# Performance work log

Hardware: AMD Instinct MI355X
Metric: run time of the kernel (lower is better)

The kernel has to match this reference:

```python
import jax, jax.numpy as jnp
import numpy as np

N = 50000
E = 1600000
D = 128
BN_EPS = 1e-5


def setup_inputs() -> dict:
    key = jax.random.key(0)
    ks = jax.random.split(key, 6)
    feature = jax.random.normal(ks[0], (N, D), dtype=jnp.float32)
    snorm_n = jax.random.uniform(ks[1], (N, 1), dtype=jnp.float32)
    src = jax.random.randint(ks[2], (E,), 0, N, dtype=jnp.int64)
    dst = jax.random.randint(ks[3], (E,), 0, N, dtype=jnp.int64)
    W = jax.random.normal(ks[4], (D, D), dtype=jnp.float32) * (1.0 / np.sqrt(D))
    b = jax.random.normal(ks[5], (D,), dtype=jnp.float32) * 0.01
    gamma = jnp.ones((D,), dtype=jnp.float32)
    beta = jnp.zeros((D,), dtype=jnp.float32)
    return {"feature": feature, "snorm_n": snorm_n, "src": src, "dst": dst,
            "W": W, "b": b, "gamma": gamma, "beta": beta}


def reference(feature, snorm_n, src, dst, W, b, gamma, beta):
    # --- copy_src + mean reduce (DGL update_all) ---
    msg = feature[src]                                    # [E, D] gather
    agg = jax.ops.segment_sum(msg, dst, num_segments=N)   # [N, D] scatter-add
    deg = jax.ops.segment_sum(jnp.ones((src.shape[0],), feature.dtype), dst,
                              num_segments=N)             # [N]
    has_msg = deg > 0
    mean = agg / jnp.maximum(deg, 1.0)[:, None]
    # nodes with no incoming edges keep their original 'h' (DGL semantics)
    h = jnp.where(has_msg[:, None], mean, feature)
    # --- apply_nodes: linear ---
    h = h @ W.T + b
    # --- graph norm ---
    h = h * snorm_n
    # --- batch norm (training-mode stats, biased variance, eps=1e-5) ---
    mu = jnp.mean(h, axis=0)
    var = jnp.mean((h - mu) ** 2, axis=0)
    h = (h - mu) / jnp.sqrt(var + BN_EPS) * gamma + beta
    # --- activation + residual (dropout p=0 -> identity) ---
    h = jax.nn.relu(h)
    h = feature + h
    return h
```

## Files before the change

### kernel.cpp

```cpp
#include <hip/hip_runtime.h>

#define D 128
#define BN_EPS 1e-5f
#define ROWS 16
#define CHUNK 4096
#define CAP_SCAN 512

typedef unsigned int u32;
typedef unsigned short u16;

__device__ inline u32 pk_bf16(float x, float y) {
    u32 ux = __float_as_uint(x), uy = __float_as_uint(y);
    ux = (ux + 0x7fffu + ((ux >> 16) & 1u)) >> 16;
    uy = (uy + 0x7fffu + ((uy >> 16) & 1u)) >> 16;
    return ux | (uy << 16);
}

__global__ __launch_bounds__(256) void cast_transpose(const float* __restrict__ feat,
                                                      u16* __restrict__ feat16,
                                                      const float* __restrict__ W,
                                                      float* __restrict__ Wt,
                                                      int ncast) {
    int b = blockIdx.x;
    if (b < ncast) {
        size_t i = ((size_t)b * 256 + threadIdx.x) * 8;
        float4 f0 = *reinterpret_cast<const float4*>(feat + i);
        float4 f1 = *reinterpret_cast<const float4*>(feat + i + 4);
        uint4 o;
        o.x = pk_bf16(f0.x, f0.y);
        o.y = pk_bf16(f0.z, f0.w);
        o.z = pk_bf16(f1.x, f1.y);
        o.w = pk_bf16(f1.z, f1.w);
        *reinterpret_cast<uint4*>(feat16 + i) = o;
    } else {
        int i = (b - ncast) * 256 + threadIdx.x;
        int r = i >> 7, c = i & 127;
        Wt[c * D + r] = W[i];
    }
}

__global__ __launch_bounds__(256) void passA(const int* __restrict__ dst,
                                             int* __restrict__ blkcnt,
                                             int nch, int nedges) {
    __shared__ int cnt[256];
    cnt[threadIdx.x] = 0;
    __syncthreads();
    const int e0 = blockIdx.x * CHUNK;
    for (int r = 0; r < CHUNK / 256; ++r) {
        int e = e0 + r * 256 + threadIdx.x;
        if (e < nedges) atomicAdd(&cnt[dst[e] >> 8], 1);
    }
    __syncthreads();
    blkcnt[(size_t)threadIdx.x * nch + blockIdx.x] = cnt[threadIdx.x];
}

__global__ __launch_bounds__(CAP_SCAN) void scanB1(int* __restrict__ blkcnt,
                                                   int* __restrict__ gtot,
                                                   int nch) {
    __shared__ int s[CAP_SCAN];
    const int t = threadIdx.x;
    const size_t row = (size_t)blockIdx.x * nch;
    int v = (t < nch) ? blkcnt[row + t] : 0;
    s[t] = v;
    __syncthreads();
    for (int off = 1; off < CAP_SCAN; off <<= 1) {
        int u = (t >= off) ? s[t - off] : 0;
        __syncthreads();
        s[t] += u;
        __syncthreads();
    }
    if (t < nch) blkcnt[row + t] = s[t] - v;
    if (t == 0) gtot[blockIdx.x] = s[CAP_SCAN - 1];
}

__global__ __launch_bounds__(256) void scanB2(const int* __restrict__ gtot,
                                              int* __restrict__ bucket_base,
                                              int* __restrict__ bucket_cnt) {
    __shared__ int s[256];
    const int t = threadIdx.x;
    int v = gtot[t];
    s[t] = v;
    __syncthreads();
    for (int off = 1; off < 256; off <<= 1) {
        int u = (t >= off) ? s[t - off] : 0;
        __syncthreads();
        s[t] += u;
        __syncthreads();
    }
    bucket_base[t] = s[t] - v;
    bucket_cnt[t] = v;
}

__global__ __launch_bounds__(256) void passB(const int* __restrict__ src,
                                             const int* __restrict__ dst,
                                             const int* __restrict__ blkcnt,
                                             const int* __restrict__ bucket_base,
                                             u32* __restrict__ gpacked,
                                             int nch, int nedges) {
    __shared__ int cnt[256];
    __shared__ int gbase[256];
    const int t = threadIdx.x;
    gbase[t] = blkcnt[(size_t)t * nch + blockIdx.x] + bucket_base[t];
    cnt[t] = 0;
    __syncthreads();
    const int e0 = blockIdx.x * CHUNK;
    for (int r = 0; r < CHUNK / 256; ++r) {
        int e = e0 + r * 256 + t;
        if (e < nedges) {
            int d = dst[e];
            int b = d >> 8;
            int pos = atomicAdd(&cnt[b], 1);
            gpacked[gbase[b] + pos] = (u32)src[e] | ((u32)(d & 255) << 16);
        }
    }
}

__global__ __launch_bounds__(256) void pass2(const u32* __restrict__ gpacked,
                                             const int* __restrict__ bucket_base,
                                             const int* __restrict__ bucket_cnt,
                                             u16* __restrict__ epos,
                                             int* __restrict__ count,
                                             int* __restrict__ offs,
                                             int nnodes) {
    __shared__ int cnt[256], lo[256], cur[256];
    const int t = threadIdx.x;
    const int b = blockIdx.x;
    const int nE = bucket_cnt[b];
    const int base = bucket_base[b];
    cnt[t] = 0;
    __syncthreads();
    for (int i = t; i < nE; i += 256) atomicAdd(&cnt[gpacked[base + i] >> 16], 1);
    __syncthreads();
    int v = cnt[t];
    lo[t] = v;
    __syncthreads();
    for (int off = 1; off < 256; off <<= 1) {
        int u = (t >= off) ? lo[t - off] : 0;
        __syncthreads();
        lo[t] += u;
        __syncthreads();
    }
    int excl = lo[t] - v;
    int n = (b << 8) + t;
    if (n < nnodes) { count[n] = v; offs[n] = base + excl; }
    cur[t] = excl;
    __syncthreads();
    for (int i = t; i < nE; i += 256) {
        u32 p = gpacked[base + i];
        int pos = atomicAdd(&cur[p >> 16], 1);
        epos[base + pos] = (u16)(p & 0xffffu);
    }
}

__global__ __launch_bounds__(256, 6) void fused_agg_linear(
        const float* __restrict__ feat,
        const u16* __restrict__ feat16,
        const float* __restrict__ snorm,
        const int* __restrict__ offs,
        const int* __restrict__ count,
        const u16* __restrict__ epos,
        const float* __restrict__ Wt,
        const float* __restrict__ bias,
        float* __restrict__ y,
        float* __restrict__ partial) {
    __shared__ float hs[ROWS][D];
    const int row0 = blockIdx.x * ROWS;
    const int wid = threadIdx.x >> 6;
    const int lane = threadIdx.x & 63;
    const int q = lane >> 4;
    const int ql = lane & 15;

#define LDB(s) (*reinterpret_cast<const uint4*>(feat16 + (size_t)(s) * D + 8 * ql))
#define ADD8(a, u) { \
    a[0] += __uint_as_float((u).x << 16); a[1] += __uint_as_float((u).x & 0xffff0000u); \
    a[2] += __uint_as_float((u).y << 16); a[3] += __uint_as_float((u).y & 0xffff0000u); \
    a[4] += __uint_as_float((u).z << 16); a[5] += __uint_as_float((u).z & 0xffff0000u); \
    a[6] += __uint_as_float((u).w << 16); a[7] += __uint_as_float((u).w & 0xffff0000u); }

    for (int rr = 0; rr < 4; ++rr) {
        const int r = wid * 4 + rr;
        const int n = row0 + r;
        const int dg = count[n];
        const int o = offs[n];
        float a0[8], a1[8];
        #pragma unroll
        for (int k = 0; k < 8; ++k) { a0[k] = 0.0f; a1[k] = 0.0f; }

        for (int base = 0; base < dg; base += 64) {
            const int m = min(64, dg - base);
            int myidx = (lane < m) ? (int)epos[o + base + lane] : 0;
            int j = 0;
            for (; j + 8 <= m; j += 8) {
                int s0 = __shfl(myidx, j + q, 64);
                int s1 = __shfl(myidx, j + 4 + q, 64);
                uint4 u0 = LDB(s0);
                uint4 u1 = LDB(s1);
                ADD8(a0, u0);
                ADD8(a1, u1);
            }
            if (j + 4 <= m) {
                int s0 = __shfl(myidx, j + q, 64);
                uint4 u0 = LDB(s0);
                ADD8(a0, u0);
                j += 4;
            }
            int rem = m - j;
            if (rem) {
                int s0 = __shfl(myidx, j + (q < rem ? q : 0), 64);
                if (q < rem) { uint4 u0 = LDB(s0); ADD8(a1, u0); }
            }
        }

        float av[8];
        #pragma unroll
        for (int k = 0; k < 8; ++k) {
            float v = a0[k] + a1[k];
            v += __shfl_xor(v, 16, 64);
            v += __shfl_xor(v, 32, 64);
            av[k] = v;
        }
        if (dg > 0) {
            float inv = 1.0f / (float)dg;
            #pragma unroll
            for (int k = 0; k < 8; ++k) av[k] *= inv;
        } else {
            float4 f0 = *reinterpret_cast<const float4*>(feat + (size_t)n * D + 8 * ql);
            float4 f1 = *reinterpret_cast<const float4*>(feat + (size_t)n * D + 8 * ql + 4);
            av[0] = f0.x; av[1] = f0.y; av[2] = f0.z; av[3] = f0.w;
            av[4] = f1.x; av[5] = f1.y; av[6] = f1.z; av[7] = f1.w;
        }
        if (q == 0) {
            *reinterpret_cast<float4*>(&hs[r][8 * ql]) = make_float4(av[0], av[1], av[2], av[3]);
            *reinterpret_cast<float4*>(&hs[r][8 * ql + 4]) = make_float4(av[4], av[5], av[6], av[7]);
        }
    }
#undef LDB
#undef ADD8
    __syncthreads();

    const int d = threadIdx.x & 127;
    const int half2 = threadIdx.x >> 7;
    float acc[8];
    #pragma unroll
    for (int r = 0; r < 8; ++r) acc[r] = 0.0f;

    for (int k = 0; k < D; k += 4) {
        float w0 = Wt[(k + 0) * D + d];
        float w1 = Wt[(k + 1) * D + d];
        float w2 = Wt[(k + 2) * D + d];
        float w3 = Wt[(k + 3) * D + d];
        #pragma unroll
        for (int r = 0; r < 8; ++r) {
            float4 h4 = *reinterpret_cast<const float4*>(&hs[half2 * 8 + r][k]);
            acc[r] += h4.x * w0 + h4.y * w1 + h4.z * w2 + h4.w * w3;
        }
    }

    const float bb = bias[d];
    float psum = 0.0f, psq = 0.0f;
    #pragma unroll
    for (int r = 0; r < 8; ++r) {
        const int n = row0 + half2 * 8 + r;
        float v = (acc[r] + bb) * snorm[n];
        y[(size_t)n * D + d] = v;
        psum += v;
        psq += v * v;
    }
    __syncthreads();
    if (half2 == 1) { hs[0][d] = psum; hs[1][d] = psq; }
    __syncthreads();
    if (half2 == 0) {
        psum += hs[0][d];
        psq += hs[1][d];
        partial[(size_t)blockIdx.x * 256 + d] = psum;
        partial[(size_t)blockIdx.x * 256 + 128 + d] = psq;
    }
}

__global__ __launch_bounds__(256) void bn_reduce(const float* __restrict__ partial,
                                                 const float* __restrict__ gamma,
                                                 const float* __restrict__ beta,
                                                 float* __restrict__ bnparam,
                                                 int nchunk, float inv_n) {
    const int d = blockIdx.x;
    float s = 0.0f, q = 0.0f;
    for (int b = threadIdx.x; b < nchunk; b += 256) {
        s += partial[(size_t)b * 256 + d];
        q += partial[(size_t)b * 256 + 128 + d];
    }
    for (int off = 32; off > 0; off >>= 1) {
        s += __shfl_down(s, off, 64);
        q += __shfl_down(q, off, 64);
    }
    __shared__ float ss[4], qq[4];
    int wid = threadIdx.x >> 6;
    int lane = threadIdx.x & 63;
    if (lane == 0) { ss[wid] = s; qq[wid] = q; }
    __syncthreads();
    if (threadIdx.x == 0) {
        float S = ss[0] + ss[1] + ss[2] + ss[3];
        float Q = qq[0] + qq[1] + qq[2] + qq[3];
        float mu = S * inv_n;
        float var = Q * inv_n - mu * mu;
        var = fmaxf(var, 0.0f);
        float rstd = rsqrtf(var + BN_EPS);
        float scale = gamma[d] * rstd;
        float shift = beta[d] - mu * scale;
        bnparam[d] = scale;
        bnparam[D + d] = shift;
    }
}

__global__ __launch_bounds__(256) void finalize(const float* __restrict__ feat,
                                                float* __restrict__ y,
                                                const float* __restrict__ bnparam,
                                                int total4) {
    int i = blockIdx.x * 256 + threadIdx.x;
    if (i >= total4) return;
    int c = i & 31;
    float4 v = reinterpret_cast<float4*>(y)[i];
    float4 f = reinterpret_cast<const float4*>(feat)[i];
    float4 sc = reinterpret_cast<const float4*>(bnparam)[c];
    float4 sh = reinterpret_cast<const float4*>(bnparam + D)[c];
    v.x = f.x + fmaxf(v.x * sc.x + sh.x, 0.0f);
    v.y = f.y + fmaxf(v.y * sc.y + sh.y, 0.0f);
    v.z = f.z + fmaxf(v.z * sc.z + sh.z, 0.0f);
    v.w = f.w + fmaxf(v.w * sc.w + sh.w, 0.0f);
    reinterpret_cast<float4*>(y)[i] = v;
}

extern "C" void kernel_launch(void* const* d_in, const int* in_sizes, int n_in,
                              void* d_out, int out_size, void* d_ws, size_t ws_size,
                              hipStream_t stream) {
    const float* feat  = (const float*)d_in[0];
    const float* snorm = (const float*)d_in[1];
    const int*   src   = (const int*)d_in[2];
    const int*   dst   = (const int*)d_in[3];
    const float* W     = (const float*)d_in[4];
    const float* bias  = (const float*)d_in[5];
    const float* gamma = (const float*)d_in[6];
    const float* beta  = (const float*)d_in[7];

    const int N = in_sizes[1];
    const int E = in_sizes[2];
    const int nblk = N / ROWS;
    const int nch = (E + CHUNK - 1) / CHUNK;
    const int nbuck = (N + 255) >> 8;
    const int ncast = (N * D) / (8 * 256);

    int* count       = (int*)d_ws;
    int* offs        = count + N;
    int* blkcnt      = offs + N;
    int* gtot        = blkcnt + (size_t)256 * nch;
    int* bucket_base = gtot + 256;
    int* bucket_cnt  = bucket_base + 256;
    u32* gpacked     = (u32*)(bucket_cnt + 256);
    u16* epos        = (u16*)(gpacked + E);
    u16* feat16      = epos + E;
    float* Wt        = (float*)(feat16 + (size_t)N * D);
    float* partial   = Wt + D * D;
    float* bnparam   = partial + (size_t)nblk * 256;

    float* y = (float*)d_out;

    cast_transpose<<<ncast + 64, 256, 0, stream>>>(feat, feat16, W, Wt, ncast);

    passA<<<nch, 256, 0, stream>>>(dst, blkcnt, nch, E);
    scanB1<<<256, CAP_SCAN, 0, stream>>>(blkcnt, gtot, nch);
    scanB2<<<1, 256, 0, stream>>>(gtot, bucket_base, bucket_cnt);
    passB<<<nch, 256, 0, stream>>>(src, dst, blkcnt, bucket_base, gpacked, nch, E);
    pass2<<<nbuck, 256, 0, stream>>>(gpacked, bucket_base, bucket_cnt,
                                     epos, count, offs, N);

    fused_agg_linear<<<nblk, 256, 0, stream>>>(feat, feat16, snorm, offs, count,
                                               epos, Wt, bias, y, partial);

    bn_reduce<<<D, 256, 0, stream>>>(partial, gamma, beta, bnparam,
                                     nblk, 1.0f / (float)N);

    {
        int total4 = N * D / 4;
        finalize<<<(total4 + 255) / 256, 256, 0, stream>>>(feat, y, bnparam, total4);
    }
}
```

Before: 159.1 us.

## Fuse bucket counting into prep kernel, widen sort passes, unroll gather further

Merges the destination-bucket counting pass into the cast/transpose kernel so one launch does both, removing a kernel boundary. Doubles the edge chunk size and halves the scan block, and runs passB and pass2 with 512 threads per block. Widens the gather loop in the aggregation kernel to four independent accumulators, putting more loads in flight per wave. The extra accumulators raise register pressure under the existing occupancy bound.

```diff
diff --git a/kernel.cpp b/kernel.cpp
--- a/kernel.cpp
+++ b/kernel.cpp
@@ -3,8 +3,8 @@
 #define D 128
 #define BN_EPS 1e-5f
 #define ROWS 16
-#define CHUNK 4096
-#define CAP_SCAN 512
+#define CHUNK 8192
+#define CAP_SCAN 256
 
 typedef unsigned int u32;
 typedef unsigned short u16;
@@ -16,12 +16,15 @@
     return ux | (uy << 16);
 }
 
-__global__ __launch_bounds__(256) void cast_transpose(const float* __restrict__ feat,
-                                                      u16* __restrict__ feat16,
-                                                      const float* __restrict__ W,
-                                                      float* __restrict__ Wt,
-                                                      int ncast) {
-    int b = blockIdx.x;
+__global__ __launch_bounds__(256) void prep(const float* __restrict__ feat,
+                                            u16* __restrict__ feat16,
+                                            const float* __restrict__ W,
+                                            float* __restrict__ Wt,
+                                            const int* __restrict__ dst,
+                                            int* __restrict__ blkcnt,
+                                            int ncast, int nch, int nedges) {
+    __shared__ int cnt[256];
+    const int b = blockIdx.x;
     if (b < ncast) {
         size_t i = ((size_t)b * 256 + threadIdx.x) * 8;
         float4 f0 = *reinterpret_cast<const float4*>(feat + i);
@@ -32,26 +35,22 @@
         o.z = pk_bf16(f1.x, f1.y);
         o.w = pk_bf16(f1.z, f1.w);
         *reinterpret_cast<uint4*>(feat16 + i) = o;
-    } else {
+    } else if (b < ncast + 64) {
         int i = (b - ncast) * 256 + threadIdx.x;
         int r = i >> 7, c = i & 127;
         Wt[c * D + r] = W[i];
-    }
-}
-
-__global__ __launch_bounds__(256) void passA(const int* __restrict__ dst,
-                                             int* __restrict__ blkcnt,
-                                             int nch, int nedges) {
-    __shared__ int cnt[256];
-    cnt[threadIdx.x] = 0;
-    __syncthreads();
-    const int e0 = blockIdx.x * CHUNK;
-    for (int r = 0; r < CHUNK / 256; ++r) {
-        int e = e0 + r * 256 + threadIdx.x;
-        if (e < nedges) atomicAdd(&cnt[dst[e] >> 8], 1);
-    }
-    __syncthreads();
-    blkcnt[(size_t)threadIdx.x * nch + blockIdx.x] = cnt[threadIdx.x];
+    } else {
+        const int c = b - ncast - 64;
+        cnt[threadIdx.x] = 0;
+        __syncthreads();
+        const int e0 = c * CHUNK;
+        for (int r = 0; r < CHUNK / 256; ++r) {
+            int e = e0 + r * 256 + threadIdx.x;
+            if (e < nedges) atomicAdd(&cnt[dst[e] >> 8], 1);
+        }
+        __syncthreads();
+        blkcnt[(size_t)threadIdx.x * nch + c] = cnt[threadIdx.x];
+    }
 }
 
 __global__ __launch_bounds__(CAP_SCAN) void scanB1(int* __restrict__ blkcnt,
@@ -91,7 +90,7 @@
     bucket_cnt[t] = v;
 }
 
-__global__ __launch_bounds__(256) void passB(const int* __restrict__ src,
+__global__ __launch_bounds__(512) void passB(const int* __restrict__ src,
                                              const int* __restrict__ dst,
                                              const int* __restrict__ blkcnt,
                                              const int* __restrict__ bucket_base,
@@ -100,12 +99,14 @@
     __shared__ int cnt[256];
     __shared__ int gbase[256];
     const int t = threadIdx.x;
-    gbase[t] = blkcnt[(size_t)t * nch + blockIdx.x] + bucket_base[t];
-    cnt[t] = 0;
+    if (t < 256) {
+        gbase[t] = blkcnt[(size_t)t * nch + blockIdx.x] + bucket_base[t];
+        cnt[t] = 0;
+    }
     __syncthreads();
     const int e0 = blockIdx.x * CHUNK;
-    for (int r = 0; r < CHUNK / 256; ++r) {
-        int e = e0 + r * 256 + t;
+    for (int r = 0; r < CHUNK / 512; ++r) {
+        int e = e0 + r * 512 + t;
         if (e < nedges) {
             int d = dst[e];
             int b = d >> 8;
@@ -115,7 +116,7 @@
     }
 }
 
-__global__ __launch_bounds__(256) void pass2(const u32* __restrict__ gpacked,
+__global__ __launch_bounds__(512) void pass2(const u32* __restrict__ gpacked,
                                              const int* __restrict__ bucket_base,
                                              const int* __restrict__ bucket_cnt,
                                              u16* __restrict__ epos,
@@ -127,25 +128,27 @@
     const int b = blockIdx.x;
     const int nE = bucket_cnt[b];
     const int base = bucket_base[b];
-    cnt[t] = 0;
-    __syncthreads();
-    for (int i = t; i < nE; i += 256) atomicAdd(&cnt[gpacked[base + i] >> 16], 1);
-    __syncthreads();
-    int v = cnt[t];
-    lo[t] = v;
+    if (t < 256) cnt[t] = 0;
+    __syncthreads();
+    for (int i = t; i < nE; i += 512) atomicAdd(&cnt[gpacked[base + i] >> 16], 1);
+    __syncthreads();
+    int v = (t < 256) ? cnt[t] : 0;
+    if (t < 256) lo[t] = v;
     __syncthreads();
     for (int off = 1; off < 256; off <<= 1) {
-        int u = (t >= off) ? lo[t - off] : 0;
-        __syncthreads();
-        lo[t] += u;
-        __syncthreads();
-    }
-    int excl = lo[t] - v;
-    int n = (b << 8) + t;
-    if (n < nnodes) { count[n] = v; offs[n] = base + excl; }
-    cur[t] = excl;
-    __syncthreads();
-    for (int i = t; i < nE; i += 256) {
+        int u = (t >= off && t < 256) ? lo[t - off] : 0;
+        __syncthreads();
+        if (t < 256) lo[t] += u;
+        __syncthreads();
+    }
+    if (t < 256) {
+        int excl = lo[t] - v;
+        int n = (b << 8) + t;
+        if (n < nnodes) { count[n] = v; offs[n] = base + excl; }
+        cur[t] = excl;
+    }
+    __syncthreads();
+    for (int i = t; i < nE; i += 512) {
         u32 p = gpacked[base + i];
         int pos = atomicAdd(&cur[p >> 16], 1);
         epos[base + pos] = (u16)(p & 0xffffu);
@@ -182,27 +185,32 @@
         const int n = row0 + r;
         const int dg = count[n];
         const int o = offs[n];
-        float a0[8], a1[8];
+        float a0[8], a1[8], a2[8], a3[8];
         #pragma unroll
-        for (int k = 0; k < 8; ++k) { a0[k] = 0.0f; a1[k] = 0.0f; }
+        for (int k = 0; k < 8; ++k) { a0[k] = 0.0f; a1[k] = 0.0f; a2[k] = 0.0f; a3[k] = 0.0f; }
 
         for (int base = 0; base < dg; base += 64) {
             const int m = min(64, dg - base);
             int myidx = (lane < m) ? (int)epos[o + base + lane] : 0;
             int j = 0;
-            for (; j + 8 <= m; j += 8) {
+            for (; j + 16 <= m; j += 16) {
                 int s0 = __shfl(myidx, j + q, 64);
                 int s1 = __shfl(myidx, j + 4 + q, 64);
+                int s2 = __shfl(myidx, j + 8 + q, 64);
+                int s3 = __shfl(myidx, j + 12 + q, 64);
                 uint4 u0 = LDB(s0);
                 uint4 u1 = LDB(s1);
+                uint4 u2 = LDB(s2);
+                uint4 u3 = LDB(s3);
                 ADD8(a0, u0);
                 ADD8(a1, u1);
+                ADD8(a2, u2);
+                ADD8(a3, u3);
             }
-            if (j + 4 <= m) {
+            for (; j + 4 <= m; j += 4) {
                 int s0 = __shfl(myidx, j + q, 64);
                 uint4 u0 = LDB(s0);
                 ADD8(a0, u0);
-                j += 4;
             }
             int rem = m - j;
             if (rem) {
@@ -214,7 +222,7 @@
         float av[8];
         #pragma unroll
         for (int k = 0; k < 8; ++k) {
-            float v = a0[k] + a1[k];
+            float v = (a0[k] + a1[k]) + (a2[k] + a3[k]);
             v += __shfl_xor(v, 16, 64);
             v += __shfl_xor(v, 32, 64);
             av[k] = v;
@@ -363,13 +371,15 @@
 
     float* y = (float*)d_out;
 
-    cast_transpose<<<ncast + 64, 256, 0, stream>>>(feat, feat16, W, Wt, ncast);
-
-    passA<<<nch, 256, 0, stream>>>(dst, blkcnt, nch, E);
+    prep<<<ncast + 64 + nch, 256, 0, stream>>>(feat, feat16, W, Wt, dst,
+                                               blkcnt, ncast, nch, E);
+
     scanB1<<<256, CAP_SCAN, 0, stream>>>(blkcnt, gtot, nch);
     scanB2<<<1, 256, 0, stream>>>(gtot, bucket_base, bucket_cnt);
-    passB<<<nch, 256, 0, stream>>>(src, dst, blkcnt, bucket_base, gpacked, nch, E);
-    pass2<<<nbuck, 256, 0, stream>>>(gpacked, bucket_base, bucket_cnt,
+
+    passB<<<nch, 512, 0, stream>>>(src, dst, blkcnt, bucket_base, gpacked, nch, E);
+
+    pass2<<<nbuck, 512, 0, stream>>>(gpacked, bucket_base, bucket_cnt,
                                      epos, count, offs, N);
 
     fused_agg_linear<<<nblk, 256, 0, stream>>>(feat, feat16, snorm, offs, count,
```

After: 162.6 us. 2.2% more time.
